# Performance work log

Measured on AMD Instinct MI355X. Metric: run time of the kernel, lower is better.

The kernel has to match this reference:

```python
import jax, jax.numpy as jnp
import numpy as np

B, C, N, T, H = 4, 128, 512, 16, 4
DK = C // H
SCALE = float(np.sqrt(DK) * 1.0)  # dk**0.5 * max(tau,1e-6), tau=1.0


def setup_inputs() -> dict:
    key = jax.random.key(0)
    ks = jax.random.split(key, 6)
    x = jax.random.normal(ks[0], (B, C, N, T), jnp.float32)
    Wq = jax.random.normal(ks[1], (C, C), jnp.float32) * (1.0 / np.sqrt(C))
    Wk = jax.random.normal(ks[2], (C, C), jnp.float32) * (1.0 / np.sqrt(C))
    # original init is identity; add tiny noise so it's not degenerate
    structural = jnp.eye(N, dtype=jnp.float32) + 0.01 * jax.random.normal(ks[3], (N, N), jnp.float32)
    fusion_w = jax.random.normal(ks[4], (2,), jnp.float32) * 0.5  # 1x1 conv over 2 input channels
    fusion_b = (jax.random.normal(ks[5], (), jnp.float32) * 0.1)
    return {"x": x, "Wq": Wq, "Wk": Wk, "structural": structural,
            "fusion_w": fusion_w, "fusion_b": fusion_b}


def reference(x, Wq, Wk, structural, fusion_w, fusion_b):
    # x: [B, C, N, T]. 1x1 conv == per-channel linear; arrange to [B,T,N,H,DK]
    Q = jnp.einsum('oc,bcnt->btno', Wq, x).reshape(B, T, N, H, DK)
    K = jnp.einsum('oc,bcnt->btno', Wk, x).reshape(B, T, N, H, DK)
    # scores: [B, T, H, N, N]
    scores = jnp.einsum('btnhd,btmhd->bthnm', Q, K) / SCALE
    att_node = jax.nn.softmax(scores, axis=-1).mean(axis=(1, 2))  # [B, N, N]
    att_struct = jax.nn.softmax(structural, axis=-1)              # [N, N]
    # fusion conv (1x1, 2->1 channels) == weighted sum + bias
    fused = fusion_w[0] * att_node + fusion_w[1] * att_struct[None] + fusion_b
    fused = 0.5 * (fused + jnp.swapaxes(fused, 1, 2))  # symmetrize
    fused = jax.nn.softmax(fused, axis=-1)             # normalize='softmax'
    x_bt = jnp.transpose(x, (0, 3, 2, 1))              # [B, T, N, C]
    x_att = jnp.einsum('bij,btjc->btic', fused, x_bt)  # weighted aggregation over nodes
    return jnp.transpose(x_att, (0, 3, 2, 1))          # [B, C, N, T]
```

## Files before the change

### kernel.cpp

```cpp
#include <hip/hip_runtime.h>

#define BB 4
#define CC 128
#define NN 512
#define TT 16
#define HH 4
#define DKK 32
#define GPART 4
#define INV_SCALE 0.17677669529663687f

typedef __attribute__((ext_vector_type(8))) short bf16x8;
typedef __attribute__((ext_vector_type(4))) float f32x4;

__device__ __forceinline__ unsigned int pk2bf(float a, float b) {
  unsigned int ua = __float_as_uint(a);
  ua = (ua + 0x7FFFu + ((ua >> 16) & 1u)) >> 16;
  unsigned int ub = __float_as_uint(b);
  ub = (ub + 0x7FFFu + ((ub >> 16) & 1u)) >> 16;
  return ua | (ub << 16);
}

__device__ __forceinline__ unsigned int pkfast(float a, float b) {
  unsigned int au = __float_as_uint(a) + 0x8000u;
  unsigned int bu = __float_as_uint(b) + 0x8000u;
  return __builtin_amdgcn_perm(bu, au, 0x07060302u);
}

__device__ __forceinline__ float bf2f(ushort v) {
  return __uint_as_float((unsigned int)v << 16);
}

__global__ __launch_bounds__(256) void k_proj(const float* __restrict__ x,
                                              const float* __restrict__ Wq,
                                              const float* __restrict__ Wk,
                                              ushort* __restrict__ Qb,
                                              ushort* __restrict__ Kb,
                                              ushort* __restrict__ xtb) {
  __shared__ float xl[128 * 66];
  const int b = blockIdx.y;
  const int nt0 = blockIdx.x * 64;
  const int nq = nt0 >> 4;
  const int tid = threadIdx.x;
  const int w = tid >> 6, lane = tid & 63;
  const int lm = lane & 15, quad = lane >> 4;

  const float* xb = x + (size_t)b * 1048576 + nt0;
#pragma unroll
  for (int L = tid * 4; L < 8192; L += 1024) {
    int c = L >> 6, j = L & 63;
    float4 v = *(const float4*)(xb + c * 8192 + j);
    float2* dp = (float2*)(xl + c * 66 + j);
    dp[0] = make_float2(v.x, v.y);
    dp[1] = make_float2(v.z, v.w);
  }

  const int o0 = w * 32;
  bf16x8 aq[2][4], ak[2][4];
#pragma unroll
  for (int ot = 0; ot < 2; ++ot)
#pragma unroll
    for (int kc = 0; kc < 4; ++kc) {
      const int off = (o0 + ot * 16 + lm) * 128 + kc * 32 + quad * 8;
      const float4 q1 = *(const float4*)(Wq + off);
      const float4 q2 = *(const float4*)(Wq + off + 4);
      const float4 k1 = *(const float4*)(Wk + off);
      const float4 k2 = *(const float4*)(Wk + off + 4);
      union { uint4 u; bf16x8 v; } cq, ck;
      cq.u.x = pk2bf(q1.x * INV_SCALE, q1.y * INV_SCALE);
      cq.u.y = pk2bf(q1.z * INV_SCALE, q1.w * INV_SCALE);
      cq.u.z = pk2bf(q2.x * INV_SCALE, q2.y * INV_SCALE);
      cq.u.w = pk2bf(q2.z * INV_SCALE, q2.w * INV_SCALE);
      ck.u.x = pk2bf(k1.x, k1.y);
      ck.u.y = pk2bf(k1.z, k1.w);
      ck.u.z = pk2bf(k2.x, k2.y);
      ck.u.w = pk2bf(k2.z, k2.w);
      aq[ot][kc] = cq.v;
      ak[ot][kc] = ck.v;
    }
  __syncthreads();

#pragma unroll
  for (int jtl = 0; jtl < 4; ++jtl) {
    bf16x8 bfr[4];
#pragma unroll
    for (int kc = 0; kc < 4; ++kc) {
      const float* sp = xl + (kc * 32 + quad * 8) * 66 + jtl * 16 + lm;
      float f0 = sp[0],   f1 = sp[66],  f2 = sp[132], f3 = sp[198];
      float f4 = sp[264], f5 = sp[330], f6 = sp[396], f7 = sp[462];
      union { uint4 u; bf16x8 v; } cv;
      cv.u.x = pkfast(f0, f1);
      cv.u.y = pkfast(f2, f3);
      cv.u.z = pkfast(f4, f5);
      cv.u.w = pkfast(f6, f7);
      bfr[kc] = cv.v;
    }

    f32x4 accq0 = {0,0,0,0}, accq1 = {0,0,0,0};
    f32x4 acck0 = {0,0,0,0}, acck1 = {0,0,0,0};
#pragma unroll
    for (int kc = 0; kc < 4; ++kc) {
      accq0 = __builtin_amdgcn_mfma_f32_16x16x32_bf16(aq[0][kc], bfr[kc], accq0, 0, 0, 0);
      accq1 = __builtin_amdgcn_mfma_f32_16x16x32_bf16(aq[1][kc], bfr[kc], accq1, 0, 0, 0);
      acck0 = __builtin_amdgcn_mfma_f32_16x16x32_bf16(ak[0][kc], bfr[kc], acck0, 0, 0, 0);
      acck1 = __builtin_amdgcn_mfma_f32_16x16x32_bf16(ak[1][kc], bfr[kc], acck1, 0, 0, 0);
    }

    const size_t base = (size_t)b * 1048576 + (size_t)lm * 65536 + w * 16384 +
                        (size_t)(nq + jtl) * 32 + quad * 4;
    uint2 uq0, uq1, uk0, uk1;
    uq0.x = pk2bf(accq0[0], accq0[1]); uq0.y = pk2bf(accq0[2], accq0[3]);
    uq1.x = pk2bf(accq1[0], accq1[1]); uq1.y = pk2bf(accq1[2], accq1[3]);
    uk0.x = pk2bf(acck0[0], acck0[1]); uk0.y = pk2bf(acck0[2], acck0[3]);
    uk1.x = pk2bf(acck1[0], acck1[1]); uk1.y = pk2bf(acck1[2], acck1[3]);
    *(uint2*)(Qb + base)      = uq0;
    *(uint2*)(Qb + base + 16) = uq1;
    *(uint2*)(Kb + base)      = uk0;
    *(uint2*)(Kb + base + 16) = uk1;
  }

  const int tloc = tid & 15, c0 = (tid >> 4) * 8;
  ushort* xo = xtb + ((size_t)b * 128) * 8192;
#pragma unroll
  for (int s = 0; s < 8; ++s) {
    const int c = c0 + s;
    const float* sp = xl + c * 66 + tloc;
    uint2 u;
    u.x = pk2bf(sp[0], sp[16]);
    u.y = pk2bf(sp[32], sp[48]);
    *(uint2*)(xo + (size_t)c * 8192 + tloc * 512 + nq) = u;
  }
}

__global__ __launch_bounds__(256, 4) void k_scores(const ushort* __restrict__ Qb,
                                                   const ushort* __restrict__ Kb,
                                                   ushort* __restrict__ part) {
  __shared__ float SH[16 * 516];
  __shared__ float red[2][4][16];
  const int strip = blockIdx.x, g = blockIdx.y, b = blockIdx.z;
  const int tid = threadIdx.x;
  const int w = tid >> 6, lane = tid & 63;
  const int lm = lane & 15, quad = lane >> 4;
  const int n0 = strip * 16;
  const int wcol0 = w * 128;

  float acc[32];
#pragma unroll
  for (int i = 0; i < 32; ++i) acc[i] = 0.f;

  for (int pi = 0; pi < 16; ++pi) {
    const int p = g * 16 + pi;
    const size_t base = (size_t)((b * 16 + (p >> 2)) * 4 + (p & 3)) * 16384;
    bf16x8 afrag = *(const bf16x8*)(Qb + base + (size_t)(n0 + lm) * 32 + quad * 8);
    bf16x8 bfr[8];
#pragma unroll
    for (int ct = 0; ct < 8; ++ct)
      bfr[ct] = *(const bf16x8*)(Kb + base + (size_t)(wcol0 + ct * 16 + lm) * 32 + quad * 8);

    f32x4 d[8];
#pragma unroll
    for (int ct = 0; ct < 8; ++ct) {
      f32x4 z = {0.f, 0.f, 0.f, 0.f};
      d[ct] = __builtin_amdgcn_mfma_f32_16x16x32_bf16(afrag, bfr[ct], z, 0, 0, 0);
    }

    float cur[32];
    float rp0 = 0.f, rp1 = 0.f, rp2 = 0.f, rp3 = 0.f;
#pragma unroll
    for (int ct = 0; ct < 8; ++ct) {
      float e0 = __expf(d[ct][0]);
      float e1 = __expf(d[ct][1]);
      float e2 = __expf(d[ct][2]);
      float e3 = __expf(d[ct][3]);
      cur[ct * 4 + 0] = e0; cur[ct * 4 + 1] = e1;
      cur[ct * 4 + 2] = e2; cur[ct * 4 + 3] = e3;
      rp0 += e0; rp1 += e1; rp2 += e2; rp3 += e3;
    }
#pragma unroll
    for (int m = 1; m < 16; m <<= 1) {
      rp0 += __shfl_xor(rp0, m);
      rp1 += __shfl_xor(rp1, m);
      rp2 += __shfl_xor(rp2, m);
      rp3 += __shfl_xor(rp3, m);
    }
    if (lm == 0) {
      red[pi & 1][w][quad * 4 + 0] = rp0;
      red[pi & 1][w][quad * 4 + 1] = rp1;
      red[pi & 1][w][quad * 4 + 2] = rp2;
      red[pi & 1][w][quad * 4 + 3] = rp3;
    }
    __syncthreads();
#pragma unroll
    for (int r = 0; r < 4; ++r) {
      float rs = red[pi & 1][0][quad * 4 + r] + red[pi & 1][1][quad * 4 + r] +
                 red[pi & 1][2][quad * 4 + r] + red[pi & 1][3][quad * 4 + r];
      float inv = 1.0f / rs;
#pragma unroll
      for (int ct = 0; ct < 8; ++ct)
        acc[ct * 4 + r] = fmaf(cur[ct * 4 + r], inv, acc[ct * 4 + r]);
    }
  }

#pragma unroll
  for (int ct = 0; ct < 8; ++ct) {
#pragma unroll
    for (int r = 0; r < 4; ++r)
      SH[(quad * 4 + r) * 516 + wcol0 + ct * 16 + lm] = acc[ct * 4 + r];
  }
  __syncthreads();
  const int row = tid >> 4, colb = (tid & 15) * 4;
  ushort* po = part + ((size_t)((g * 4 + b) * 512 + n0 + row)) * 512 + colb;
#pragma unroll
  for (int k = 0; k < 8; ++k) {
    f32x4 v = *(const f32x4*)(SH + row * 516 + colb + k * 64);
    uint2 u;
    u.x = pk2bf(v[0], v[1]);
    u.y = pk2bf(v[2], v[3]);
    *(uint2*)(po + k * 64) = u;
  }
}

__device__ __forceinline__ float blk_max(float v, float* red, int tid) {
#pragma unroll
  for (int off = 32; off > 0; off >>= 1) v = fmaxf(v, __shfl_xor(v, off, 64));
  if ((tid & 63) == 0) red[tid >> 6] = v;
  __syncthreads();
  v = fmaxf(fmaxf(red[0], red[1]), fmaxf(red[2], red[3]));
  __syncthreads();
  return v;
}
__device__ __forceinline__ float blk_sum(float v, float* red, int tid) {
#pragma unroll
  for (int off = 32; off > 0; off >>= 1) v += __shfl_xor(v, off, 64);
  if ((tid & 63) == 0) red[tid >> 6] = v;
  __syncthreads();
  v = (red[0] + red[1]) + (red[2] + red[3]);
  __syncthreads();
  return v;
}

__global__ __launch_bounds__(256) void k_struct(const float* __restrict__ S,
                                                float* __restrict__ st) {
  __shared__ float red[4];
  const int i = blockIdx.x, tid = threadIdx.x;
  float s0 = S[i * 512 + tid], s1 = S[i * 512 + tid + 256];
  float m = blk_max(fmaxf(s0, s1), red, tid);
  float e0 = __expf(s0 - m), e1 = __expf(s1 - m);
  float sum = blk_sum(e0 + e1, red, tid);
  float inv = 1.0f / sum;
  st[i * 512 + tid] = e0 * inv;
  st[i * 512 + tid + 256] = e1 * inv;
}

__global__ __launch_bounds__(256) void k_redsym(const ushort* __restrict__ part,
                                                float* __restrict__ Ssym,
                                                float* __restrict__ st) {
  __shared__ float L1[64 * 68];
  __shared__ float L2[64 * 68];
  const int z = blockIdx.y;
  int rem = blockIdx.x, ti = 0;
  for (;;) { int cnt = 8 - ti; if (rem < cnt) break; rem -= cnt; ++ti; }
  const int tj = ti + rem;
  const bool diag = (ti == tj);
  const int tid = threadIdx.x;
  const int rr = tid >> 2, cc = (tid & 3) * 16;

  float a1[16], a2[16];
#pragma unroll
  for (int k = 0; k < 16; ++k) { a1[k] = 0.f; a2[k] = 0.f; }

  if (z == 4) {
    const float* p1 = st + (ti * 64 + rr) * 512 + tj * 64 + cc;
    const float* p2 = st + (tj * 64 + rr) * 512 + ti * 64 + cc;
#pragma unroll
    for (int q = 0; q < 4; ++q) {
      float4 v = *(const float4*)(p1 + q * 4);
      a1[q * 4 + 0] = v.x; a1[q * 4 + 1] = v.y;
      a1[q * 4 + 2] = v.z; a1[q * 4 + 3] = v.w;
      if (!diag) {
        float4 u = *(const float4*)(p2 + q * 4);
        a2[q * 4 + 0] = u.x; a2[q * 4 + 1] = u.y;
        a2[q * 4 + 2] = u.z; a2[q * 4 + 3] = u.w;
      }
    }
  } else {
    const int b = z;
#pragma unroll
    for (int g = 0; g < GPART; ++g) {
      const ushort* p1 = part + ((size_t)((g * 4 + b) * 512 + ti * 64 + rr)) * 512 + tj * 64 + cc;
      const ushort* p2 = part + ((size_t)((g * 4 + b) * 512 + tj * 64 + rr)) * 512 + ti * 64 + cc;
#pragma unroll
      for (int q = 0; q < 4; ++q) {
        ushort4 v = *(const ushort4*)(p1 + q * 4);
        a1[q * 4 + 0] += bf2f(v.x); a1[q * 4 + 1] += bf2f(v.y);
        a1[q * 4 + 2] += bf2f(v.z); a1[q * 4 + 3] += bf2f(v.w);
        if (!diag) {
          ushort4 u = *(const ushort4*)(p2 + q * 4);
          a2[q * 4 + 0] += bf2f(u.x); a2[q * 4 + 1] += bf2f(u.y);
          a2[q * 4 + 2] += bf2f(u.z); a2[q * 4 + 3] += bf2f(u.w);
        }
      }
    }
  }

#pragma unroll
  for (int q = 0; q < 4; ++q) {
    *(float4*)(L1 + rr * 68 + cc + q * 4) =
        make_float4(a1[q * 4], a1[q * 4 + 1], a1[q * 4 + 2], a1[q * 4 + 3]);
    if (!diag)
      *(float4*)(L2 + rr * 68 + cc + q * 4) =
          make_float4(a2[q * 4], a2[q * 4 + 1], a2[q * 4 + 2], a2[q * 4 + 3]);
  }
  __syncthreads();

  float* M = (z < 4) ? (Ssym + (size_t)z * 262144) : st;
  const float* LT = diag ? L1 : L2;
#pragma unroll
  for (int q = 0; q < 4; ++q) {
    const int c = cc + q * 4;
    float4 o;
    o.x = L1[rr * 68 + c + 0] + LT[(c + 0) * 68 + rr];
    o.y = L1[rr * 68 + c + 1] + LT[(c + 1) * 68 + rr];
    o.z = L1[rr * 68 + c + 2] + LT[(c + 2) * 68 + rr];
    o.w = L1[rr * 68 + c + 3] + LT[(c + 3) * 68 + rr];
    *(float4*)(M + (ti * 64 + rr) * 512 + tj * 64 + c) = o;
  }
  if (!diag) {
#pragma unroll
    for (int q = 0; q < 4; ++q) {
      const int c = cc + q * 4;
      float4 o;
      o.x = L2[rr * 68 + c + 0] + L1[(c + 0) * 68 + rr];
      o.y = L2[rr * 68 + c + 1] + L1[(c + 1) * 68 + rr];
      o.z = L2[rr * 68 + c + 2] + L1[(c + 2) * 68 + rr];
      o.w = L2[rr * 68 + c + 3] + L1[(c + 3) * 68 + rr];
      *(float4*)(M + (tj * 64 + rr) * 512 + ti * 64 + c) = o;
    }
  }
}

__global__ __launch_bounds__(256) void k_fused(const float* __restrict__ Ssym,
                                               const float* __restrict__ st,
                                               const float* __restrict__ fw,
                                               const float* __restrict__ fb,
                                               ushort* __restrict__ fusedb) {
  __shared__ float red[4];
  const int i = blockIdx.x, b = blockIdx.y, tid = threadIdx.x;
  const float w0s = fw[0] * (0.5f / 64.f);
  const float w1s = fw[1] * 0.5f;
  const float bias = fb[0];
  const float* A = Ssym + (size_t)b * 262144 + (size_t)i * 512;
  const float* S = st + (size_t)i * 512;
  float2 a2 = *(const float2*)(A + tid * 2);
  float2 s2 = *(const float2*)(S + tid * 2);
  float l0 = fmaf(w0s, a2.x, fmaf(w1s, s2.x, bias));
  float l1 = fmaf(w0s, a2.y, fmaf(w1s, s2.y, bias));
  float m = blk_max(fmaxf(l0, l1), red, tid);
  float e0 = __expf(l0 - m), e1 = __expf(l1 - m);
  float sum = blk_sum(e0 + e1, red, tid);
  float inv = 1.0f / sum;
  *(unsigned int*)(fusedb + ((size_t)(b * 512 + i)) * 512 + tid * 2) =
      pk2bf(e0 * inv, e1 * inv);
}

__global__ __launch_bounds__(256) void k_agg(const ushort* __restrict__ fusedb,
                                             const ushort* __restrict__ xtb,
                                             float* __restrict__ out) {
  __shared__ ushort xs[16 * 520];
  const int cg = blockIdx.x;
  const int i0 = blockIdx.y * 64;
  const int b = blockIdx.z;
  const int tid = threadIdx.x, w = tid >> 6, lane = tid & 63;
  const int lm = lane & 15, quad = lane >> 4;

  const ushort* fr = fusedb + ((size_t)(b * 512 + i0 + w * 16 + lm)) * 512 + quad * 8;
  bf16x8 af[16];
#pragma unroll
  for (int kk = 0; kk < 16; ++kk) af[kk] = *(const bf16x8*)(fr + kk * 32);

  const ushort* xg = xtb + ((size_t)b * 128 + cg * 8) * 8192;
  uint4 rg[4];
#pragma unroll
  for (int it = 0; it < 4; ++it) rg[it] = *(const uint4*)(xg + (tid + it * 256) * 8);

  for (int c = 0; c < 8; ++c) {
#pragma unroll
    for (int it = 0; it < 4; ++it) {
      int u = (tid + it * 256) * 8;
      int t = u >> 9, j0 = u & 511;
      *(uint4*)(xs + t * 520 + j0) = rg[it];
    }
    __syncthreads();
    if (c < 7) {
      const ushort* xg2 = xg + (size_t)(c + 1) * 8192;
#pragma unroll
      for (int it = 0; it < 4; ++it) rg[it] = *(const uint4*)(xg2 + (tid + it * 256) * 8);
    }
    f32x4 acc = {0.f, 0.f, 0.f, 0.f};
#pragma unroll
    for (int kk = 0; kk < 16; ++kk) {
      bf16x8 bf = *(const bf16x8*)(xs + lm * 520 + kk * 32 + quad * 8);
      acc = __builtin_amdgcn_mfma_f32_16x16x32_bf16(af[kk], bf, acc, 0, 0, 0);
    }
    float* op = out + (size_t)b * 1048576 + (size_t)(cg * 8 + c) * 8192 +
                (size_t)(i0 + w * 16 + quad * 4) * 16 + lm;
    op[0]  = acc[0];
    op[16] = acc[1];
    op[32] = acc[2];
    op[48] = acc[3];
    __syncthreads();
  }
}

extern "C" void kernel_launch(void* const* d_in, const int* in_sizes, int n_in,
                              void* d_out, int out_size, void* d_ws, size_t ws_size,
                              hipStream_t stream) {
  const float* x  = (const float*)d_in[0];
  const float* Wq = (const float*)d_in[1];
  const float* Wk = (const float*)d_in[2];
  const float* S  = (const float*)d_in[3];
  const float* fw = (const float*)d_in[4];
  const float* fb = (const float*)d_in[5];
  float* out = (float*)d_out;

  ushort* Qb   = (ushort*)d_ws;
  ushort* Kb   = Qb + 4194304;
  ushort* part = Kb + 4194304;
  ushort* xtb  = part + 4194304;
  float* Ssym  = (float*)(xtb + 4194304);
  float* st    = Ssym + 1048576;
  ushort* fusedb = (ushort*)(st + 262144);

  k_proj  <<<dim3(128, 4),      256, 0, stream>>>(x, Wq, Wk, Qb, Kb, xtb);
  k_scores<<<dim3(32, GPART, 4),256, 0, stream>>>(Qb, Kb, part);
  k_struct<<<dim3(512),         256, 0, stream>>>(S, st);
  k_redsym<<<dim3(36, 5),       256, 0, stream>>>(part, Ssym, st);
  k_fused <<<dim3(512, 4),      256, 0, stream>>>(Ssym, st, fw, fb, fusedb);
  k_agg   <<<dim3(16, 8, 4),    256, 0, stream>>>(fusedb, xtb, out);
}
```

Baseline: 171.7 us.

## Double score split-K partitions and move x bf16 transpose into separate kernel

Raises GPART from 4 to 8, so k_scores launches twice as many blocks and each block loops over 8 (t,h) pairs instead of 16, writing more bf16 partial score planes for k_redsym to reduce. The x to bf16 transposed conversion is moved out of k_proj into a new k_xconv kernel that runs after k_redsym. That kernel reuses the partial-score buffer for xtb, keeping workspace use flat despite the larger partials. The aim is more parallelism in the score stage and a lighter k_proj, at the cost of an extra launch, rereading x from global memory, and more partial traffic.

New measurement: 166.6 us. -3.0%, faster.

```diff
diff --git a/kernel.cpp b/kernel.cpp
--- a/kernel.cpp
+++ b/kernel.cpp
@@ -6,7 +6,7 @@
 #define TT 16
 #define HH 4
 #define DKK 32
-#define GPART 4
+#define GPART 8
 #define INV_SCALE 0.17677669529663687f
 
 typedef __attribute__((ext_vector_type(8))) short bf16x8;
@@ -20,6 +20,11 @@
   return ua | (ub << 16);
 }
 
+__device__ __forceinline__ ushort cv1(float f) {
+  unsigned int u = __float_as_uint(f);
+  return (ushort)((u + 0x7FFFu + ((u >> 16) & 1u)) >> 16);
+}
+
 __device__ __forceinline__ unsigned int pkfast(float a, float b) {
   unsigned int au = __float_as_uint(a) + 0x8000u;
   unsigned int bu = __float_as_uint(b) + 0x8000u;
@@ -34,8 +39,7 @@
                                               const float* __restrict__ Wq,
                                               const float* __restrict__ Wk,
                                               ushort* __restrict__ Qb,
-                                              ushort* __restrict__ Kb,
-                                              ushort* __restrict__ xtb) {
+                                              ushort* __restrict__ Kb) {
   __shared__ float xl[128 * 66];
   const int b = blockIdx.y;
   const int nt0 = blockIdx.x * 64;
@@ -117,18 +121,6 @@
     *(uint2*)(Kb + base)      = uk0;
     *(uint2*)(Kb + base + 16) = uk1;
   }
-
-  const int tloc = tid & 15, c0 = (tid >> 4) * 8;
-  ushort* xo = xtb + ((size_t)b * 128) * 8192;
-#pragma unroll
-  for (int s = 0; s < 8; ++s) {
-    const int c = c0 + s;
-    const float* sp = xl + c * 66 + tloc;
-    uint2 u;
-    u.x = pk2bf(sp[0], sp[16]);
-    u.y = pk2bf(sp[32], sp[48]);
-    *(uint2*)(xo + (size_t)c * 8192 + tloc * 512 + nq) = u;
-  }
 }
 
 __global__ __launch_bounds__(256, 4) void k_scores(const ushort* __restrict__ Qb,
@@ -147,8 +139,8 @@
 #pragma unroll
   for (int i = 0; i < 32; ++i) acc[i] = 0.f;
 
-  for (int pi = 0; pi < 16; ++pi) {
-    const int p = g * 16 + pi;
+  for (int pi = 0; pi < 8; ++pi) {
+    const int p = (g << 3) + pi;
     const size_t base = (size_t)((b * 16 + (p >> 2)) * 4 + (p & 3)) * 16384;
     bf16x8 afrag = *(const bf16x8*)(Qb + base + (size_t)(n0 + lm) * 32 + quad * 8);
     bf16x8 bfr[8];
@@ -216,6 +208,33 @@
     u.x = pk2bf(v[0], v[1]);
     u.y = pk2bf(v[2], v[3]);
     *(uint2*)(po + k * 64) = u;
+  }
+}
+
+__global__ __launch_bounds__(256) void k_xconv(const float* __restrict__ x,
+                                               ushort* __restrict__ xtb) {
+  __shared__ ushort xs[16 * 520];
+  const int c = blockIdx.x, b = blockIdx.y;
+  const int tid = threadIdx.x;
+  const float* in = x + ((size_t)b * 128 + c) * 8192;
+  ushort* outp = xtb + ((size_t)b * 128 + c) * 8192;
+
+#pragma unroll
+  for (int it = 0; it < 8; ++it) {
+    int idx = (tid + it * 256) * 4;
+    int j = idx >> 4, t0 = idx & 15;
+    float4 v = *(const float4*)(in + idx);
+    xs[(t0 + 0) * 520 + j] = cv1(v.x);
+    xs[(t0 + 1) * 520 + j] = cv1(v.y);
+    xs[(t0 + 2) * 520 + j] = cv1(v.z);
+    xs[(t0 + 3) * 520 + j] = cv1(v.w);
+  }
+  __syncthreads();
+#pragma unroll
+  for (int it = 0; it < 4; ++it) {
+    int u = (tid + it * 256) * 8;
+    int t = u >> 9, j0 = u & 511;
+    *(uint4*)(outp + u) = *(const uint4*)(xs + t * 520 + j0);
   }
 }
 
@@ -425,15 +444,16 @@
   ushort* Qb   = (ushort*)d_ws;
   ushort* Kb   = Qb + 4194304;
   ushort* part = Kb + 4194304;
-  ushort* xtb  = part + 4194304;
-  float* Ssym  = (float*)(xtb + 4194304);
+  ushort* xtb  = part;
+  float* Ssym  = (float*)(part + 8388608);
   float* st    = Ssym + 1048576;
   ushort* fusedb = (ushort*)(st + 262144);
 
-  k_proj  <<<dim3(128, 4),      256, 0, stream>>>(x, Wq, Wk, Qb, Kb, xtb);
+  k_proj  <<<dim3(128, 4),      256, 0, stream>>>(x, Wq, Wk, Qb, Kb);
   k_scores<<<dim3(32, GPART, 4),256, 0, stream>>>(Qb, Kb, part);
   k_struct<<<dim3(512),         256, 0, stream>>>(S, st);
   k_redsym<<<dim3(36, 5),       256, 0, stream>>>(part, Ssym, st);
+  k_xconv <<<dim3(128, 4),      256, 0, stream>>>(x, xtb);
   k_fused <<<dim3(512, 4),      256, 0, stream>>>(Ssym, st, fw, fb, fusedb);
   k_agg   <<<dim3(16, 8, 4),    256, 0, stream>>>(fusedb, xtb, out);
 }
```
